# Optimization experiments

Measured on AMD Instinct MI355X. Metric: run time of the kernel, lower is better.

The kernel has to match this reference:

```python
import jax, jax.numpy as jnp
import numpy as np
import math

B, T, H, NH, E, W = 64, 256, 512, 8, 7, 5
DH = H // NH
NEG = -10000.0


def _ln(x, g, b, eps=1e-12):
    m = x.mean(-1, keepdims=True)
    v = ((x - m) ** 2).mean(-1, keepdims=True)
    return (x - m) / jnp.sqrt(v + eps) * g + b


def _attn(q_in, k_in, v_in, Wq, bq, Wk, bk, Wv, bv, bias):
    # q_in: [B,Tq,H], k_in/v_in: [B,Tk,H], bias broadcastable to [B,NH,Tq,Tk]
    Bq, Tq, _ = q_in.shape
    Tk = k_in.shape[1]
    q = (q_in @ Wq + bq).reshape(Bq, Tq, NH, DH)
    k = (k_in @ Wk + bk).reshape(Bq, Tk, NH, DH)
    v = (v_in @ Wv + bv).reshape(Bq, Tk, NH, DH)
    s = jnp.einsum('bqhd,bkhd->bhqk', q, k) / math.sqrt(DH) + bias
    p = jax.nn.softmax(s, axis=-1)
    ctx = jnp.einsum('bhqk,bkhd->bqhd', p, v)
    return ctx.reshape(Bq, Tq, H)


def _make_mask_biases(lengths, speakers):
    # Vectorized equivalents of get_ext_att_mask (additive -10000 biases).
    j = jnp.arange(T)[None, :, None]          # query position
    k = jnp.arange(T)[None, None, :]          # key position
    L = lengths[:, None, None]                # [B,1,1]
    row = j < L                               # valid query rows
    col = k < L                               # valid key cols
    # global: [B,1,1,T], key validity only
    bias_g = ((1.0 - col.astype(jnp.float32)) * NEG)[:, None, :, :]  # j dim acts as the size-1 axis
    # local: sliding window of width W (odd): |j-k| <= W//2, within length
    m_l = row & col & (jnp.abs(j - k) <= (W // 2))
    # intra: same-speaker keys for valid rows (columns NOT trimmed, per source)
    sp_j = speakers[:, :, None]
    sp_k = speakers[:, None, :]
    m_intra = row & (sp_k == sp_j)
    # inter: different-speaker keys for valid rows, columns trimmed to length
    m_inter = row & (sp_k != sp_j) & col
    to_bias = lambda m: ((1.0 - m.astype(jnp.float32)) * NEG)[:, None, :, :]
    return bias_g, to_bias(m_l), to_bias(m_intra), to_bias(m_inter)


def _forward(x, lengths, speakers, emo_table,
             t_Wq, t_bq, t_Wk, t_bk, t_Wv, t_bv, t_Wo, t_bo, t_ln_g, t_ln_b,
             b_Wq, b_bq, b_Wk, b_bk, b_Wv, b_bv, b_Wo, b_bo,
             W1, b1, ln2_g, ln2_b, W2):
    # Tendency attention: utterances attend to the E emotion embeddings (BertAttention)
    emo = jnp.broadcast_to(emo_table[None], (B, E, H))
    ctx = _attn(x, emo, emo, t_Wq, t_bq, t_Wk, t_bk, t_Wv, t_bv, 0.0)
    h_t = _ln(ctx @ t_Wo + t_bo + x, t_ln_g, t_ln_b)
    # Four masked self-attention branches (EmotionAttention: attn + dense, no LN)
    biases = _make_mask_biases(lengths, speakers)
    outs = []
    for i in range(4):
        c = _attn(h_t, h_t, h_t, b_Wq[i], b_bq[i], b_Wk[i], b_bk[i],
                  b_Wv[i], b_bv[i], biases[i])
        outs.append(c @ b_Wo[i] + b_bo[i])
    cat = jnp.concatenate(outs, axis=-1)          # [B,T,4H]
    h_e = _ln(cat @ W1 + b1 + h_t, ln2_g, ln2_b)  # fuse branches + residual + LN
    return h_e @ W2                                # transform2 (no bias)


def setup_inputs():
    key = jax.random.key(0)
    ks = jax.random.split(key, 16)
    nrm = lambda k, shape: jax.random.normal(k, shape, dtype=jnp.float32) * 0.02
    z = lambda *s: jnp.zeros(s, jnp.float32)
    o = lambda *s: jnp.ones(s, jnp.float32)
    return {
        'x': jax.random.normal(ks[0], (B, T, H), dtype=jnp.float32),
        'lengths': jax.random.randint(ks[1], (B,), T // 2, T + 1),
        'speakers': jax.random.randint(ks[2], (B, T), 0, 2),
        'emo_table': nrm(ks[3], (E, H)),
        't_Wq': nrm(ks[4], (H, H)), 't_bq': z(H),
        't_Wk': nrm(ks[5], (H, H)), 't_bk': z(H),
        't_Wv': nrm(ks[6], (H, H)), 't_bv': z(H),
        't_Wo': nrm(ks[7], (H, H)), 't_bo': z(H),
        't_ln_g': o(H), 't_ln_b': z(H),
        'b_Wq': nrm(ks[8], (4, H, H)), 'b_bq': z(4, H),
        'b_Wk': nrm(ks[9], (4, H, H)), 'b_bk': z(4, H),
        'b_Wv': nrm(ks[10], (4, H, H)), 'b_bv': z(4, H),
        'b_Wo': nrm(ks[11], (4, H, H)), 'b_bo': z(4, H),
        'W1': nrm(ks[12], (4 * H, H)), 'b1': z(H),
        'ln2_g': o(H), 'ln2_b': z(H),
        'W2': nrm(ks[13], (H, H)),
    }


def reference(x, lengths, speakers, emo_table,
              t_Wq, t_bq, t_Wk, t_bk, t_Wv, t_bv, t_Wo, t_bo, t_ln_g, t_ln_b,
              b_Wq, b_bq, b_Wk, b_bk, b_Wv, b_bv, b_Wo, b_bo,
              W1, b1, ln2_g, ln2_b, W2):
    return _forward(x, lengths, speakers, emo_table,
                    t_Wq, t_bq, t_Wk, t_bk, t_Wv, t_bv, t_Wo, t_bo, t_ln_g, t_ln_b,
                    b_Wq, b_bq, b_Wk, b_bk, b_Wv, b_bv, b_Wo, b_bo,
                    W1, b1, ln2_g, ln2_b, W2)
```

## Files before the change

### kernel.cpp

```cpp
#include <hip/hip_runtime.h>

#define B_  64
#define T_  256
#define H_  512
#define NH_ 8
#define DH_ 64
#define M_  16384
#define SL  262144

typedef float  f32x4 __attribute__((ext_vector_type(4)));
typedef float  f32x2 __attribute__((ext_vector_type(2)));
typedef __bf16 b16x8 __attribute__((ext_vector_type(8)));
typedef __bf16 b16x4 __attribute__((ext_vector_type(4)));
typedef __bf16 b16x2 __attribute__((ext_vector_type(2)));

__device__ __forceinline__ void gload16(const void* g, void* l) {
  __builtin_amdgcn_global_load_lds((const __attribute__((address_space(1))) void*)g,
                                   (__attribute__((address_space(3))) void*)l, 16, 0, 0);
}

__global__ __launch_bounds__(256) void cvt_f32_bf16_k(const float* __restrict__ in,
                                                      __bf16* __restrict__ out) {
  size_t i = ((size_t)blockIdx.x * 256 + threadIdx.x) * 4;
  f32x4 v = *(const f32x4*)(in + i);
  b16x4 o;
  o[0] = (__bf16)v[0]; o[1] = (__bf16)v[1]; o[2] = (__bf16)v[2]; o[3] = (__bf16)v[3];
  *(b16x4*)(out + i) = o;
}

struct TP15 { const float* src[15]; int slot[15]; float scl[15]; };
__global__ __launch_bounds__(256) void transpose_cvt15(TP15 p, __bf16* __restrict__ wT) {
  __shared__ float tile[32][33];
  const float* in = p.src[blockIdx.z];
  __bf16* out = wT + (size_t)p.slot[blockIdx.z] * SL;
  const float scl = p.scl[blockIdx.z];
  int c0 = blockIdx.x * 32, r0 = blockIdx.y * 32;
  int tx = threadIdx.x & 31, ty = threadIdx.x >> 5;
  for (int yy = ty; yy < 32; yy += 8)
    tile[yy][tx] = in[(size_t)(r0 + yy) * 512 + c0 + tx];
  __syncthreads();
  for (int yy = ty; yy < 32; yy += 8)
    out[(size_t)(c0 + yy) * 512 + r0 + tx] = (__bf16)(tile[tx][yy] * scl);
}

__global__ __launch_bounds__(256) void transpose_cvt(const float* __restrict__ in,
                                                     __bf16* __restrict__ out, int R, int C) {
  __shared__ float tile[32][33];
  int c0 = blockIdx.x * 32, r0 = blockIdx.y * 32;
  int tx = threadIdx.x & 31, ty = threadIdx.x >> 5;
  for (int yy = ty; yy < 32; yy += 8)
    tile[yy][tx] = in[(size_t)(r0 + yy) * C + c0 + tx];
  __syncthreads();
  for (int yy = ty; yy < 32; yy += 8)
    out[(size_t)(c0 + yy) * R + r0 + tx] = (__bf16)tile[tx][yy];
}

__global__ __launch_bounds__(512) void emo_kv(const float* __restrict__ emo,
                                              const float* __restrict__ Wk, const float* __restrict__ bk,
                                              const float* __restrict__ Wv, const float* __restrict__ bv,
                                              float* __restrict__ kout, float* __restrict__ vout) {
  int e = blockIdx.x, n = threadIdx.x;
  const float* W = blockIdx.y ? Wv : Wk;
  const float* bb = blockIdx.y ? bv : bk;
  float* o = blockIdx.y ? vout : kout;
  float acc = 0.f;
  for (int kk = 0; kk < 512; ++kk) acc += emo[e * 512 + kk] * W[kk * 512 + n];
  o[e * 512 + n] = acc + bb[n];
}

__global__ __launch_bounds__(512) void sentprep(const float* __restrict__ Wq,
                                                const float* __restrict__ bq,
                                                const float* __restrict__ Wo,
                                                const float* __restrict__ kemo,
                                                const float* __restrict__ vemo,
                                                __bf16* __restrict__ Wqk_bf,
                                                __bf16* __restrict__ VWo_bf,
                                                float* __restrict__ sbias) {
  const int he = blockIdx.x, h = he / 7, e = he % 7;
  const int t = threadIdx.x;
  const float* kp = kemo + e * 512 + h * 64;
  const float* wqr = Wq + (size_t)t * 512 + h * 64;
  float a = 0.f;
#pragma unroll 8
  for (int d = 0; d < 64; ++d) a += wqr[d] * kp[d];
  Wqk_bf[he * 512 + t] = (__bf16)(a * 0.125f);
  const float* vp = vemo + e * 512 + h * 64;
  float v = 0.f;
#pragma unroll 8
  for (int d = 0; d < 64; ++d) v += vp[d] * Wo[(size_t)(h * 64 + d) * 512 + t];
  VWo_bf[t * 64 + h * 8 + e] = (__bf16)v;
  if (e == 0) VWo_bf[t * 64 + h * 8 + 7] = (__bf16)0.f;
  if (t == 0) {
    float s = 0.f;
    for (int d = 0; d < 64; ++d) s += bq[h * 64 + d] * kp[d];
    sbias[he] = s * 0.125f;
  }
}

__global__ __launch_bounds__(512) void sentpad(__bf16* __restrict__ Wqk_bf,
                                               float* __restrict__ sbias) {
  int r = 56 + blockIdx.x;
  Wqk_bf[r * 512 + threadIdx.x] = (__bf16)0.f;
  if (threadIdx.x == 0) sbias[r] = 0.f;
}

__global__ __launch_bounds__(512) void concat_qk_bias(const float* __restrict__ bq,
                                                      const float* __restrict__ bk,
                                                      float* __restrict__ out) {
  int i = blockIdx.x, t = threadIdx.x;
  int base = (i >> 1) * 2048 + (i & 1) * 1024;
  out[base + t]       = bq[i * 512 + t];
  out[base + 512 + t] = bk[i * 512 + t] * 0.125f;
}

__global__ __launch_bounds__(256) void bias2_p1(const float* __restrict__ bo,
                                                const float* __restrict__ W1,
                                                float* __restrict__ partial) {
  int p = blockIdx.x, t = threadIdx.x;
  float a0 = 0.f, a1 = 0.f;
  for (int g = p * 128; g < p * 128 + 128; ++g) {
    float bg = bo[g];
    a0 += bg * W1[(size_t)g * 512 + t];
    a1 += bg * W1[(size_t)g * 512 + 256 + t];
  }
  partial[p * 512 + t] = a0;
  partial[p * 512 + 256 + t] = a1;
}

__global__ __launch_bounds__(256) void bias2_p2(const float* __restrict__ b1,
                                                const float* __restrict__ partial,
                                                float* __restrict__ out) {
  int o = blockIdx.x * 256 + threadIdx.x;
  float acc = b1[o];
#pragma unroll
  for (int p = 0; p < 16; ++p) acc += partial[p * 512 + o];
  out[o] = acc;
}

template<bool OB, int BM, int SW>
__global__ __launch_bounds__(512, 2) void gemm32(const __bf16* __restrict__ A,
                                                 const __bf16* __restrict__ Bt,
                                                 const float* __restrict__ bias,
                                                 void* __restrict__ Cv,
                                                 int N, int K, int lda, int ldc) {
  __shared__ __attribute__((aligned(16))) __bf16 As[2][256 * 32];
  __shared__ __attribute__((aligned(16))) __bf16 Bs[2][128 * 32];
  const int gx = gridDim.x;
  const int bid = blockIdx.y * gx + blockIdx.x;
  int bx, by;
  if (SW == 0) {
    const int nwg = gx * gridDim.y;
    const int cpx = nwg >> 3;
    const int swz = (bid & 7) * cpx + (bid >> 3);
    bx = swz % gx; by = swz / gx;
  } else {
    const int gxc = gx >> 3;
    const int u = bid >> 3, c = bid & 7;
    bx = c * gxc + u % gxc;
    by = u / gxc;
  }
  const int tid = threadIdx.x, lane = tid & 63, wid = tid >> 6;
  const int wr = wid >> 2, wc = wid & 3;
  const int m0 = by * 256, n0 = bx * 128;
  const int l15 = lane & 15, l16 = lane >> 4;
  const int ra = tid >> 2;
  const int xsl = (tid & 3) ^ ((ra >> 1) & 3);
  const int nt = K >> 5;
  f32x4 acc[8][2] = {};

#define STAGE32(buf, k0)                                                             \
  { char* aw = (char*)&As[buf][0];                                                   \
    char* bw = (char*)&Bs[buf][0];                                                   \
    gload16(A + (size_t)(m0 + ra) * lda + (k0) + xsl * 8, aw + tid * 16);            \
    gload16(A + (size_t)(m0 + 128 + ra) * lda + (k0) + xsl * 8, aw + (512 + tid) * 16); \
    gload16(Bt + (size_t)(n0 + ra) * K + (k0) + xsl * 8, bw + tid * 16); }

#define CMP32(buf)                                                                   \
  { const char* Ac = (const char*)&As[buf][0];                                       \
    const char* Bc = (const char*)&Bs[buf][0];                                       \
    const int swb = ((l16 ^ ((l15 >> 1) & 3)) << 4);                                 \
    b16x8 af[8], bf[2];                                                              \
    _Pragma("unroll")                                                                \
    for (int m = 0; m < 8; ++m)                                                      \
      af[m] = *(const b16x8*)(Ac + (wr * 128 + m * 16 + l15) * 64 + swb);            \
    _Pragma("unroll")                                                                \
    for (int n = 0; n < 2; ++n)                                                      \
      bf[n] = *(const b16x8*)(Bc + (wc * 32 + n * 16 + l15) * 64 + swb);             \
    __builtin_amdgcn_s_setprio(1);                                                   \
    _Pragma("unroll")                                                                \
    for (int m = 0; m < 8; ++m)                                                      \
      _Pragma("unroll")                                                              \
      for (int n = 0; n < 2; ++n)                                                    \
        acc[m][n] = __builtin_amdgcn_mfma_f32_16x16x32_bf16(af[m], bf[n], acc[m][n], 0, 0, 0); \
    __builtin_amdgcn_s_setprio(0); }

  STAGE32(0, 0);
  int cur = 0;
  for (int t = 0; t < nt; ++t) {
    if (t + 1 < nt) {
      STAGE32(cur ^ 1, (t + 1) * 32);
      asm volatile("s_waitcnt vmcnt(3)" ::: "memory");
    } else {
      asm volatile("s_waitcnt vmcnt(0)" ::: "memory");
    }
    __builtin_amdgcn_s_barrier();
    CMP32(cur);
    asm volatile("s_waitcnt lgkmcnt(0)" ::: "memory");
    __builtin_amdgcn_s_barrier();
    cur ^= 1;
  }
#undef STAGE32
#undef CMP32

  const int rb = m0 + wr * 128 + l16 * 4;
  const int cb = n0 + wc * 32 + l15;
#pragma unroll
  for (int n = 0; n < 2; ++n) {
    int gc = cb + n * 16;
    float bc = (BM == 1) ? bias[gc] : 0.0f;
#pragma unroll
    for (int m = 0; m < 8; ++m) {
#pragma unroll
      for (int rr = 0; rr < 4; ++rr) {
        int gr = rb + m * 16 + rr;
        float val = acc[m][n][rr] + ((BM == 2) ? bias[gr] : bc);
        if (OB) ((__bf16*)Cv)[(size_t)gr * ldc + gc] = (__bf16)val;
        else    ((float*)Cv)[(size_t)gr * ldc + gc] = val;
      }
    }
  }
}

template<bool OB, int BM, int SW>
__global__ __launch_bounds__(256) void gemm_bt64(const __bf16* __restrict__ A,
                                                 const __bf16* __restrict__ Bt,
                                                 const float* __restrict__ bias,
                                                 void* __restrict__ Cv,
                                                 int N, int K, int lda, int ldc,
                                                 size_t zA, size_t zB, size_t zC) {
  __shared__ __attribute__((aligned(16))) __bf16 As[128 * 32];
  __shared__ __attribute__((aligned(16))) __bf16 Bs[64 * 32];
  A  += (size_t)blockIdx.z * zA;
  Bt += (size_t)blockIdx.z * zB;
  char* Cb = (char*)Cv + (size_t)blockIdx.z * zC * (OB ? 2 : 4);
  const int gx = gridDim.x;
  const int bid = blockIdx.y * gx + blockIdx.x;
  int bx, by;
  if (SW == 0) {
    const int nwg = gx * gridDim.y;
    const int cpx = nwg >> 3;
    const int swz = (bid & 7) * cpx + (bid >> 3);
    bx = swz % gx; by = swz / gx;
  } else {
    const int gxc = gx >> 3;
    const int u = bid >> 3, c = bid & 7;
    bx = c * gxc + u % gxc;
    by = u / gxc;
  }
  const int tid = threadIdx.x, lane = tid & 63, wid = tid >> 6;
  const int m0 = by * 128, n0 = bx * 64;
  const int l15 = lane & 15, l16 = lane >> 4;
  const int r0 = tid >> 2, o0 = (tid & 3) * 8;
  const __bf16* a0 = A + (size_t)(m0 + r0) * lda + o0;
  const __bf16* a1 = A + (size_t)(m0 + 64 + r0) * lda + o0;
  const __bf16* bp0 = Bt + (size_t)(n0 + r0) * K + o0;
  char* AsW = (char*)As + wid * 1024;
  char* BsW = (char*)Bs + wid * 1024;
  f32x4 acc[2][4] = {};
  for (int k0 = 0; k0 < K; k0 += 32) {
    gload16(a0 + k0, AsW);
    gload16(a1 + k0, AsW + 4096);
    gload16(bp0 + k0, BsW);
    __syncthreads();
    b16x8 af[2], bf[4];
#pragma unroll
    for (int m = 0; m < 2; ++m) af[m] = *(const b16x8*)&As[(wid * 32 + m * 16 + l15) * 32 + l16 * 8];
#pragma unroll
    for (int n = 0; n < 4; ++n) bf[n] = *(const b16x8*)&Bs[(n * 16 + l15) * 32 + l16 * 8];
#pragma unroll
    for (int m = 0; m < 2; ++m)
#pragma unroll
      for (int n = 0; n < 4; ++n)
        acc[m][n] = __builtin_amdgcn_mfma_f32_16x16x32_bf16(af[m], bf[n], acc[m][n], 0, 0, 0);
    __syncthreads();
  }
  const int rbase = m0 + wid * 32 + l16 * 4;
  const int cb = n0 + l15;
#pragma unroll
  for (int n = 0; n < 4; ++n) {
    int gc = cb + n * 16;
    float bc = (BM == 1) ? bias[gc] : 0.0f;
#pragma unroll
    for (int m = 0; m < 2; ++m) {
#pragma unroll
      for (int rr = 0; rr < 4; ++rr) {
        int gr = rbase + m * 16 + rr;
        float val = acc[m][n][rr] + ((BM == 2) ? bias[gr] : bc);
        if (OB) ((__bf16*)Cb)[(size_t)gr * ldc + gc] = (__bf16)val;
        else    ((float*)Cb)[(size_t)gr * ldc + gc] = val;
      }
    }
  }
}

__global__ __launch_bounds__(256) void softmax7(const float* __restrict__ scores,
                                                __bf16* __restrict__ P) {
  int idx = blockIdx.x * 256 + threadIdx.x;
  int m = idx >> 3, h = idx & 7;
  const float* s = scores + (size_t)m * 64 + h * 7;
  float v[7], mx = -3.4e38f;
#pragma unroll
  for (int e = 0; e < 7; ++e) { v[e] = s[e]; mx = fmaxf(mx, v[e]); }
  float sum = 0.f;
#pragma unroll
  for (int e = 0; e < 7; ++e) { v[e] = __expf(v[e] - mx); sum += v[e]; }
  float inv = 1.f / sum;
  __bf16* o = P + (size_t)m * 64 + h * 8;
#pragma unroll
  for (int e = 0; e < 7; ++e) o[e] = (__bf16)(v[e] * inv);
  o[7] = (__bf16)0.f;
}

__global__ __launch_bounds__(256) void ln1_bf(const __bf16* __restrict__ pre,
                                              const float* __restrict__ res,
                                              const float* __restrict__ g,
                                              const float* __restrict__ bt,
                                              __bf16* __restrict__ ob) {
  int row = blockIdx.x, t = threadIdx.x;
  size_t base = (size_t)row * 512;
  b16x2 p2 = *(const b16x2*)(pre + base + 2 * t);
  f32x2 r2 = *(const f32x2*)(res + base + 2 * t);
  float v0 = (float)p2[0] + r2[0];
  float v1 = (float)p2[1] + r2[1];
  float s = v0 + v1, q = v0 * v0 + v1 * v1;
#pragma unroll
  for (int off = 32; off; off >>= 1) { s += __shfl_xor(s, off); q += __shfl_xor(q, off); }
  __shared__ float ls[4], lq[4];
  int wid = t >> 6, lane = t & 63;
  if (lane == 0) { ls[wid] = s; lq[wid] = q; }
  __syncthreads();
  s = ls[0] + ls[1] + ls[2] + ls[3];
  q = lq[0] + lq[1] + lq[2] + lq[3];
  float mean = s * (1.f / 512.f);
  float var = q * (1.f / 512.f) - mean * mean;
  float rstd = rsqrtf(fmaxf(var, 0.f) + 1e-12f);
  b16x2 o;
  o[0] = (__bf16)((v0 - mean) * rstd * g[2 * t] + bt[2 * t]);
  o[1] = (__bf16)((v1 - mean) * rstd * g[2 * t + 1] + bt[2 * t + 1]);
  *(b16x2*)(ob + base + 2 * t) = o;
}

__global__ __launch_bounds__(256) void ln2_bb(const __bf16* __restrict__ pre,
                                              const __bf16* __restrict__ res,
                                              const float* __restrict__ g,
                                              const float* __restrict__ bt,
                                              __bf16* __restrict__ ob) {
  int row = blockIdx.x, t = threadIdx.x;
  size_t base = (size_t)row * 512;
  b16x2 p2 = *(const b16x2*)(pre + base + 2 * t);
  b16x2 r2 = *(const b16x2*)(res + base + 2 * t);
  float v0 = (float)p2[0] + (float)r2[0];
  float v1 = (float)p2[1] + (float)r2[1];
  float s = v0 + v1, q = v0 * v0 + v1 * v1;
#pragma unroll
  for (int off = 32; off; off >>= 1) { s += __shfl_xor(s, off); q += __shfl_xor(q, off); }
  __shared__ float ls[4], lq[4];
  int wid = t >> 6, lane = t & 63;
  if (lane == 0) { ls[wid] = s; lq[wid] = q; }
  __syncthreads();
  s = ls[0] + ls[1] + ls[2] + ls[3];
  q = lq[0] + lq[1] + lq[2] + lq[3];
  float mean = s * (1.f / 512.f);
  float var = q * (1.f / 512.f) - mean * mean;
  float rstd = rsqrtf(fmaxf(var, 0.f) + 1e-12f);
  b16x2 o;
  o[0] = (__bf16)((v0 - mean) * rstd * g[2 * t] + bt[2 * t]);
  o[1] = (__bf16)((v1 - mean) * rstd * g[2 * t + 1] + bt[2 * t + 1]);
  *(b16x2*)(ob + base + 2 * t) = o;
}

template<int PAIR>
__global__ __launch_bounds__(256, 4) void attn_branch(const __bf16* __restrict__ qk,
                                                      const __bf16* __restrict__ vt,
                                                      __bf16* __restrict__ ctx,
                                                      const int* __restrict__ lengths,
                                                      const int* __restrict__ speakers) {
  __shared__ __attribute__((aligned(16))) __bf16 Ks[256 * 64];
  __shared__ __attribute__((aligned(16))) __bf16 Ps[32 * 264];
  __shared__ float redS[2][32];
  __shared__ int spk[256];
  const int sqk = 2048, so = 2048;
  const int tid = threadIdx.x, lane = tid & 63, wid = tid >> 6;
  const int l15 = lane & 15, l16 = lane >> 4;
  const int bh = blockIdx.x, z = blockIdx.y;
  const int BR = PAIR * 2 + z;
  const int b = bh >> 3, h = bh & 7;
  const int wq = wid & 1, wk = wid >> 1;
  const int mh = wid & 1, nh = wid >> 1;
  const __bf16* qp = qk + z * 1024;
  const __bf16* kp = qp + 512;
  const __bf16* vb2 = vt + (size_t)(BR * 512 + h * DH_) * M_ + b * T_;
  __bf16* ctxp = ctx + (size_t)BR * 512;
  const __bf16 CB = (__bf16)10000.0f, mCB = (__bf16)(-10000.0f), ZB = (__bf16)0.0f, OB1 = (__bf16)1.0f;
  const float CBF = (float)CB;
  const float MSTAR = (BR == 1) ? 16.0f : CBF + 16.0f;

  {
    const size_t kb0 = (size_t)(b * T_) * sqk + h * DH_;
    const int rsub = lane >> 3, slot = lane & 7;
#pragma unroll
    for (int j = 0; j < 8; ++j) {
      int row = (j * 4 + wid) * 8 + rsub;
      gload16(kp + kb0 + (size_t)row * sqk + ((slot ^ (row & 7)) * 8),
              (char*)Ks + (j * 4 + wid) * 1024);
    }
  }
  spk[tid] = speakers[b * T_ + tid];
  __syncthreads();
  const int L = lengths[b];

  b16x8 af0, af1;
  {
    const __bf16* qr = qp + (size_t)(b * T_ + wq * 16 + l15) * sqk + h * DH_;
    af0 = *(const b16x8*)(qr + l16 * 8);
    af1 = *(const b16x8*)(qr + 32 + l16 * 8);
  }

  for (int qc = 0; qc < 8; ++qc) {
    const int q0 = qc * 32;
    b16x8 afU = {};
    if (BR != 1 && l16 == 0) {
      int jA = q0 + wq * 16 + l15;
      bool rv = jA < L;
      afU[0] = rv ? OB1 : ZB;
      afU[1] = (rv && spk[jA]) ? OB1 : ZB;
      afU[2] = (BR == 0) ? OB1 : (rv ? ZB : OB1);
    }

    f32x4 sa[4][2] = {};
#pragma unroll
    for (int kc = 0; kc < 4; ++kc) {
#pragma unroll
      for (int nn = 0; nn < 2; ++nn) {
        int krw = kc * 64 + wk * 32 + nn * 16 + l15;
        b16x8 b0 = *(const b16x8*)((char*)Ks + krw * 128 + ((l16 ^ (krw & 7)) * 16));
        sa[kc][nn] = __builtin_amdgcn_mfma_f32_16x16x32_bf16(af0, b0, sa[kc][nn], 0, 0, 0);
        b16x8 b1 = *(const b16x8*)((char*)Ks + krw * 128 + (((4 + l16) ^ (krw & 7)) * 16));
        sa[kc][nn] = __builtin_amdgcn_mfma_f32_16x16x32_bf16(af1, b1, sa[kc][nn], 0, 0, 0);
        if (BR != 1) {
          b16x8 w = {};
          if (l16 == 0) {
            bool cv = krw < L;
            int sc = spk[krw];
            if (BR == 0) {
              w[2] = cv ? CB : ZB;
            } else if (BR == 2) {
              w[0] = sc ? ZB : CB;
              w[1] = sc ? CB : mCB;
              w[2] = CB;
            } else {
              w[0] = (cv && sc) ? CB : ZB;
              w[1] = cv ? (sc ? mCB : CB) : ZB;
              w[2] = CB;
            }
          }
          sa[kc][nn] = __builtin_amdgcn_mfma_f32_16x16x32_bf16(afU, w, sa[kc][nn], 0, 0, 0);
        }
      }
    }

    if (qc + 1 < 8) {
      const __bf16* qr = qp + (size_t)(b * T_ + (qc + 1) * 32 + wq * 16 + l15) * sqk + h * DH_;
      af0 = *(const b16x8*)(qr + l16 * 8);
      af1 = *(const b16x8*)(qr + 32 + l16 * 8);
    }

    const int rloc = wq * 16 + l16 * 4;
    float sm[4];
#pragma unroll
    for (int rr = 0; rr < 4; ++rr) {
      const int j = q0 + rloc + rr;
      const bool rv = j < L;
      float s = 0.f;
#pragma unroll
      for (int kc = 0; kc < 4; ++kc)
#pragma unroll
        for (int nn = 0; nn < 2; ++nn) {
          float v = sa[kc][nn][rr];
          if (BR == 1) {
            int c = kc * 64 + wk * 32 + nn * 16 + l15;
            int dj = j - c;
            bool ok = (c < L) && (dj <= 2) && (dj >= -2);
            v += (ok || !rv) ? 0.0f : -10000.0f;
          }
          float e = __expf(v - MSTAR);
          sa[kc][nn][rr] = e;
          s += e;
        }
      s += __shfl_xor(s, 1); s += __shfl_xor(s, 2); s += __shfl_xor(s, 4); s += __shfl_xor(s, 8);
      sm[rr] = s;
    }
#pragma unroll
    for (int rr = 0; rr < 4; ++rr) {
      if (l15 == 0) redS[wk][rloc + rr] = sm[rr];
#pragma unroll
      for (int kc = 0; kc < 4; ++kc)
#pragma unroll
        for (int nn = 0; nn < 2; ++nn)
          Ps[(rloc + rr) * 264 + kc * 64 + wk * 32 + nn * 16 + l15] = (__bf16)sa[kc][nn][rr];
    }
    __syncthreads();

    f32x4 oa[2] = {};
#pragma unroll
    for (int kt = 0; kt < 8; ++kt) {
      b16x8 afp = *(const b16x8*)(Ps + (mh * 16 + l15) * 264 + kt * 32 + l16 * 8);
#pragma unroll
      for (int n = 0; n < 2; ++n) {
        int d = nh * 32 + n * 16 + l15;
        b16x8 bfr = *(const b16x8*)(vb2 + (size_t)d * M_ + kt * 32 + l16 * 8);
        oa[n] = __builtin_amdgcn_mfma_f32_16x16x32_bf16(afp, bfr, oa[n], 0, 0, 0);
      }
    }
#pragma unroll
    for (int rr = 0; rr < 4; ++rr) {
      int row = mh * 16 + l16 * 4 + rr;
      float rinv = 1.0f / (redS[0][row] + redS[1][row]);
#pragma unroll
      for (int n = 0; n < 2; ++n)
        ctxp[(size_t)(b * T_ + q0 + row) * so + h * DH_ + nh * 32 + n * 16 + l15]
            = (__bf16)(oa[n][rr] * rinv);
    }
    __syncthreads();
  }
}

extern "C" void kernel_launch(void* const* d_in, const int* in_sizes, int n_in,
                              void* d_out, int out_size, void* d_ws, size_t ws_size,
                              hipStream_t stream) {
  const float* x        = (const float*)d_in[0];
  const int*   lengths  = (const int*)d_in[1];
  const int*   speakers = (const int*)d_in[2];
  const float* emo      = (const float*)d_in[3];
  const float* t_Wq = (const float*)d_in[4];
  const float* t_bq = (const float*)d_in[5];
  const float* t_Wk = (const float*)d_in[6];
  const float* t_bk = (const float*)d_in[7];
  const float* t_Wv = (const float*)d_in[8];
  const float* t_bv = (const float*)d_in[9];
  const float* t_Wo = (const float*)d_in[10];
  const float* t_bo = (const float*)d_in[11];
  const float* t_ln_g = (const float*)d_in[12];
  const float* t_ln_b = (const float*)d_in[13];
  const float* b_Wq = (const float*)d_in[14];
  const float* b_bq = (const float*)d_in[15];
  const float* b_Wk = (const float*)d_in[16];
  const float* b_bk = (const float*)d_in[17];
  const float* b_Wv = (const float*)d_in[18];
  const float* b_bv = (const float*)d_in[19];
  const float* b_Wo = (const float*)d_in[20];
  const float* b_bo = (const float*)d_in[21];
  const float* W1   = (const float*)d_in[22];
  const float* b1   = (const float*)d_in[23];
  const float* ln2_g = (const float*)d_in[24];
  const float* ln2_b = (const float*)d_in[25];
  const float* W2   = (const float*)d_in[26];

  if (ws_size < 232314880) return;

  char* ws = (char*)d_ws;
  __bf16* wT      = (__bf16*)(ws);
  __bf16* bWo_bf  = (__bf16*)(ws + 9437184);
  __bf16* Btbig   = (__bf16*)(ws + 11534336);
  float*  qkbias  = (float*)(ws + 13631488);
  float*  bias2   = (float*)(ws + 13647872);
  float*  kemo    = (float*)(ws + 13649920);
  float*  vemo    = (float*)(ws + 13664256);
  __bf16* Wqk_bf  = (__bf16*)(ws + 13678592);
  __bf16* VWo_bf  = (__bf16*)(ws + 13744128);
  float*  sbias   = (float*)(ws + 13809664);
  __bf16* htb     = (__bf16*)(ws + 13908224);
  __bf16* qkb2    = (__bf16*)(ws + 30685440);
  __bf16* vtb_all = (__bf16*)(ws + 97794304);
  __bf16* ctxa    = (__bf16*)(ws + 164903168);
  __bf16* xb      = (__bf16*)(ws + 164903168);
  float*  partial = (float*)(ws + 30685440);
  float*  scores  = (float*)(ws + 30685440);
  __bf16* Pmat    = (__bf16*)(ws + 30685440 + 4194304);
  __bf16* sctx    = (__bf16*)(ws + 30685440 + 8388608);
  __bf16* tmpb    = qkb2;
  __bf16* heb     = (__bf16*)(ws + 47462656);

  cvt_f32_bf16_k<<<dim3(8192), 256, 0, stream>>>(x, xb);
  cvt_f32_bf16_k<<<dim3(1024), 256, 0, stream>>>(b_Wo, bWo_bf);
  {
    TP15 p;
    const float* srcs[13] = {b_Wq, b_Wq + SL, b_Wq + 2 * SL, b_Wq + 3 * SL,
                             b_Wk, b_Wk + SL, b_Wk + 2 * SL, b_Wk + 3 * SL,
                             b_Wv, b_Wv + SL, b_Wv + 2 * SL, b_Wv + 3 * SL,
                             W2};
    const int slots[13] = {2, 4, 6, 8, 3, 5, 7, 9, 10, 11, 12, 13, 0};
    for (int i = 0; i < 13; ++i) {
      p.src[i] = srcs[i]; p.slot[i] = slots[i];
      p.scl[i] = (i >= 4 && i < 8) ? 0.125f : 1.0f;
    }
    for (int i = 13; i < 15; ++i) { p.src[i] = W2; p.slot[i] = 0; p.scl[i] = 1.0f; }
    transpose_cvt15<<<dim3(16, 16, 13), 256, 0, stream>>>(p, wT);
  }
  transpose_cvt<<<dim3(16, 64), 256, 0, stream>>>(W1, wT + 14 * SL, 2048, 512);
  emo_kv<<<dim3(7, 2), 512, 0, stream>>>(emo, t_Wk, t_bk, t_Wv, t_bv, kemo, vemo);
  concat_qk_bias<<<dim3(4), 512, 0, stream>>>(b_bq, b_bk, qkbias);
  bias2_p1<<<dim3(16), 256, 0, stream>>>(b_bo, W1, partial);
  bias2_p2<<<dim3(2), 256, 0, stream>>>(b1, partial, bias2);
  sentprep<<<dim3(56), 512, 0, stream>>>(t_Wq, t_bq, t_Wo, kemo, vemo, Wqk_bf, VWo_bf, sbias);
  sentpad<<<dim3(8), 512, 0, stream>>>(Wqk_bf, sbias);
  gemm_bt64<true, 0, 0><<<dim3(8, 4, 4), 256, 0, stream>>>(wT + 14 * SL, bWo_bf, nullptr, Btbig,
                                                           512, 512, 2048, 2048, 512, SL, 512);

  gemm_bt64<false, 1, 0><<<dim3(1, 128), 256, 0, stream>>>(xb, Wqk_bf, sbias, scores,
                                                           64, 512, 512, 64, 0, 0, 0);
  softmax7<<<dim3(512), 256, 0, stream>>>(scores, Pmat);
  gemm_bt64<true, 1, 0><<<dim3(8, 128), 256, 0, stream>>>(Pmat, VWo_bf, t_bo, sctx,
                                                          512, 64, 64, 512, 0, 0, 0);
  ln1_bf<<<dim3(16384), 256, 0, stream>>>(sctx, x, t_ln_g, t_ln_b, htb);

  gemm32<true, 2, 1><<<dim3(128, 8), 512, 0, stream>>>(wT + 10 * SL, htb, b_bv,
                                                       vtb_all, 16384, 512, 512, 16384);

  for (int p = 0; p < 2; ++p) {
    gemm32<true, 1, 0><<<dim3(16, 64), 512, 0, stream>>>(htb, wT + (2 + 4 * p) * SL, qkbias + p * 2048,
                                                         qkb2, 2048, 512, 512, 2048);
    dim3 ag(512, 2);
    if (p == 0) attn_branch<0><<<ag, 256, 0, stream>>>(qkb2, vtb_all, ctxa, lengths, speakers);
    else        attn_branch<1><<<ag, 256, 0, stream>>>(qkb2, vtb_all, ctxa, lengths, speakers);
  }

  gemm32<true, 1, 0><<<dim3(4, 64), 512, 0, stream>>>(ctxa, Btbig, bias2, tmpb, 512, 2048, 2048, 512);
  ln2_bb<<<dim3(16384), 256, 0, stream>>>(tmpb, htb, ln2_g, ln2_b, heb);
  gemm32<false, 0, 0><<<dim3(4, 64), 512, 0, stream>>>(heb, wT + 0 * SL, nullptr, (float*)d_out, 512, 512, 512, 512);
}
```

Measured before the change: 510.7 us.

## Give each wave full key rows in branch attention to drop block barriers

Restructures the branch attention kernel so each wave owns 16 query rows across all 256 keys and computes the full softmax row sum itself. This removes the cross-wave reduction through shared memory and both per-iteration __syncthreads, and gives each wave a private P buffer. Each wave now computes all 64 output head dims, so it reads V for the full head and holds 16 score accumulators in registers. The launch_bounds occupancy hint is dropped, which may raise register pressure and lower occupancy.

```diff
diff --git a/kernel.cpp b/kernel.cpp
--- a/kernel.cpp
+++ b/kernel.cpp
@@ -380,14 +380,13 @@
 }
 
 template<int PAIR>
-__global__ __launch_bounds__(256, 4) void attn_branch(const __bf16* __restrict__ qk,
-                                                      const __bf16* __restrict__ vt,
-                                                      __bf16* __restrict__ ctx,
-                                                      const int* __restrict__ lengths,
-                                                      const int* __restrict__ speakers) {
+__global__ __launch_bounds__(256) void attn_branch(const __bf16* __restrict__ qk,
+                                                   const __bf16* __restrict__ vt,
+                                                   __bf16* __restrict__ ctx,
+                                                   const int* __restrict__ lengths,
+                                                   const int* __restrict__ speakers) {
   __shared__ __attribute__((aligned(16))) __bf16 Ks[256 * 64];
-  __shared__ __attribute__((aligned(16))) __bf16 Ps[32 * 264];
-  __shared__ float redS[2][32];
+  __shared__ __attribute__((aligned(16))) __bf16 Ps[4][16 * 264];
   __shared__ int spk[256];
   const int sqk = 2048, so = 2048;
   const int tid = threadIdx.x, lane = tid & 63, wid = tid >> 6;
@@ -395,8 +394,6 @@
   const int bh = blockIdx.x, z = blockIdx.y;
   const int BR = PAIR * 2 + z;
   const int b = bh >> 3, h = bh & 7;
-  const int wq = wid & 1, wk = wid >> 1;
-  const int mh = wid & 1, nh = wid >> 1;
   const __bf16* qp = qk + z * 1024;
   const __bf16* kp = qp + 512;
   const __bf16* vb2 = vt + (size_t)(BR * 512 + h * DH_) * M_ + b * T_;
@@ -418,120 +415,109 @@
   spk[tid] = speakers[b * T_ + tid];
   __syncthreads();
   const int L = lengths[b];
+  __bf16* PsW = &Ps[wid][0];
 
   b16x8 af0, af1;
   {
-    const __bf16* qr = qp + (size_t)(b * T_ + wq * 16 + l15) * sqk + h * DH_;
+    const __bf16* qr = qp + (size_t)(b * T_ + wid * 16 + l15) * sqk + h * DH_;
     af0 = *(const b16x8*)(qr + l16 * 8);
     af1 = *(const b16x8*)(qr + 32 + l16 * 8);
   }
 
-  for (int qc = 0; qc < 8; ++qc) {
-    const int q0 = qc * 32;
+  for (int it = 0; it < 4; ++it) {
+    const int q0 = it * 64 + wid * 16;
     b16x8 afU = {};
     if (BR != 1 && l16 == 0) {
-      int jA = q0 + wq * 16 + l15;
+      int jA = q0 + l15;
       bool rv = jA < L;
       afU[0] = rv ? OB1 : ZB;
       afU[1] = (rv && spk[jA]) ? OB1 : ZB;
       afU[2] = (BR == 0) ? OB1 : (rv ? ZB : OB1);
     }
 
-    f32x4 sa[4][2] = {};
-#pragma unroll
-    for (int kc = 0; kc < 4; ++kc) {
-#pragma unroll
-      for (int nn = 0; nn < 2; ++nn) {
-        int krw = kc * 64 + wk * 32 + nn * 16 + l15;
-        b16x8 b0 = *(const b16x8*)((char*)Ks + krw * 128 + ((l16 ^ (krw & 7)) * 16));
-        sa[kc][nn] = __builtin_amdgcn_mfma_f32_16x16x32_bf16(af0, b0, sa[kc][nn], 0, 0, 0);
-        b16x8 b1 = *(const b16x8*)((char*)Ks + krw * 128 + (((4 + l16) ^ (krw & 7)) * 16));
-        sa[kc][nn] = __builtin_amdgcn_mfma_f32_16x16x32_bf16(af1, b1, sa[kc][nn], 0, 0, 0);
-        if (BR != 1) {
-          b16x8 w = {};
-          if (l16 == 0) {
-            bool cv = krw < L;
-            int sc = spk[krw];
-            if (BR == 0) {
-              w[2] = cv ? CB : ZB;
-            } else if (BR == 2) {
-              w[0] = sc ? ZB : CB;
-              w[1] = sc ? CB : mCB;
-              w[2] = CB;
-            } else {
-              w[0] = (cv && sc) ? CB : ZB;
-              w[1] = cv ? (sc ? mCB : CB) : ZB;
-              w[2] = CB;
-            }
+    f32x4 sa[16];
+#pragma unroll
+    for (int nn = 0; nn < 16; ++nn) {
+      int krw = nn * 16 + l15;
+      b16x8 b0 = *(const b16x8*)((char*)Ks + krw * 128 + ((l16 ^ (krw & 7)) * 16));
+      f32x4 zv = {};
+      zv = __builtin_amdgcn_mfma_f32_16x16x32_bf16(af0, b0, zv, 0, 0, 0);
+      b16x8 b1 = *(const b16x8*)((char*)Ks + krw * 128 + (((4 + l16) ^ (krw & 7)) * 16));
+      sa[nn] = __builtin_amdgcn_mfma_f32_16x16x32_bf16(af1, b1, zv, 0, 0, 0);
+      if (BR != 1) {
+        b16x8 w = {};
+        if (l16 == 0) {
+          bool cv = krw < L;
+          int sc = spk[krw];
+          if (BR == 0) {
+            w[2] = cv ? CB : ZB;
+          } else if (BR == 2) {
+            w[0] = sc ? ZB : CB;
+            w[1] = sc ? CB : mCB;
+            w[2] = CB;
+          } else {
+            w[0] = (cv && sc) ? CB : ZB;
+            w[1] = cv ? (sc ? mCB : CB) : ZB;
+            w[2] = CB;
           }
-          sa[kc][nn] = __builtin_amdgcn_mfma_f32_16x16x32_bf16(afU, w, sa[kc][nn], 0, 0, 0);
         }
+        sa[nn] = __builtin_amdgcn_mfma_f32_16x16x32_bf16(afU, w, sa[nn], 0, 0, 0);
       }
     }
 
-    if (qc + 1 < 8) {
-      const __bf16* qr = qp + (size_t)(b * T_ + (qc + 1) * 32 + wq * 16 + l15) * sqk + h * DH_;
+    if (it + 1 < 4) {
+      const __bf16* qr = qp + (size_t)(b * T_ + (it + 1) * 64 + wid * 16 + l15) * sqk + h * DH_;
       af0 = *(const b16x8*)(qr + l16 * 8);
       af1 = *(const b16x8*)(qr + 32 + l16 * 8);
     }
 
-    const int rloc = wq * 16 + l16 * 4;
-    float sm[4];
+    float rinv[4];
 #pragma unroll
     for (int rr = 0; rr < 4; ++rr) {
-      const int j = q0 + rloc + rr;
+      const int j = q0 + l16 * 4 + rr;
       const bool rv = j < L;
       float s = 0.f;
 #pragma unroll
-      for (int kc = 0; kc < 4; ++kc)
-#pragma unroll
-        for (int nn = 0; nn < 2; ++nn) {
-          float v = sa[kc][nn][rr];
-          if (BR == 1) {
-            int c = kc * 64 + wk * 32 + nn * 16 + l15;
-            int dj = j - c;
-            bool ok = (c < L) && (dj <= 2) && (dj >= -2);
-            v += (ok || !rv) ? 0.0f : -10000.0f;
-          }
-          float e = __expf(v - MSTAR);
-          sa[kc][nn][rr] = e;
-          s += e;
+      for (int nn = 0; nn < 16; ++nn) {
+        float v = sa[nn][rr];
+        if (BR == 1) {
+          int c = nn * 16 + l15;
+          int dj = j - c;
+          bool ok = (c < L) && (dj <= 2) && (dj >= -2);
+          v += (ok || !rv) ? 0.0f : -10000.0f;
         }
+        float e = __expf(v - MSTAR);
+        sa[nn][rr] = e;
+        s += e;
+      }
       s += __shfl_xor(s, 1); s += __shfl_xor(s, 2); s += __shfl_xor(s, 4); s += __shfl_xor(s, 8);
-      sm[rr] = s;
-    }
-#pragma unroll
-    for (int rr = 0; rr < 4; ++rr) {
-      if (l15 == 0) redS[wk][rloc + rr] = sm[rr];
-#pragma unroll
-      for (int kc = 0; kc < 4; ++kc)
-#pragma unroll
-        for (int nn = 0; nn < 2; ++nn)
-          Ps[(rloc + rr) * 264 + kc * 64 + wk * 32 + nn * 16 + l15] = (__bf16)sa[kc][nn][rr];
-    }
-    __syncthreads();
-
-    f32x4 oa[2] = {};
+      rinv[rr] = 1.0f / s;
+    }
+
+#pragma unroll
+    for (int rr = 0; rr < 4; ++rr)
+#pragma unroll
+      for (int nn = 0; nn < 16; ++nn)
+        PsW[(l16 * 4 + rr) * 264 + nn * 16 + l15] = (__bf16)sa[nn][rr];
+
+    f32x4 oa[4] = {};
 #pragma unroll
     for (int kt = 0; kt < 8; ++kt) {
-      b16x8 afp = *(const b16x8*)(Ps + (mh * 16 + l15) * 264 + kt * 32 + l16 * 8);
-#pragma unroll
-      for (int n = 0; n < 2; ++n) {
-        int d = nh * 32 + n * 16 + l15;
-        b16x8 bfr = *(const b16x8*)(vb2 + (size_t)d * M_ + kt * 32 + l16 * 8);
+      b16x8 afp = *(const b16x8*)&PsW[l15 * 264 + kt * 32 + l16 * 8];
+#pragma unroll
+      for (int n = 0; n < 4; ++n) {
+        b16x8 bfr = *(const b16x8*)(vb2 + (size_t)(n * 16 + l15) * M_ + kt * 32 + l16 * 8);
         oa[n] = __builtin_amdgcn_mfma_f32_16x16x32_bf16(afp, bfr, oa[n], 0, 0, 0);
       }
     }
 #pragma unroll
     for (int rr = 0; rr < 4; ++rr) {
-      int row = mh * 16 + l16 * 4 + rr;
-      float rinv = 1.0f / (redS[0][row] + redS[1][row]);
-#pragma unroll
-      for (int n = 0; n < 2; ++n)
-        ctxp[(size_t)(b * T_ + q0 + row) * so + h * DH_ + nh * 32 + n * 16 + l15]
-            = (__bf16)(oa[n][rr] * rinv);
-    }
-    __syncthreads();
+      int row = q0 + l16 * 4 + rr;
+#pragma unroll
+      for (int n = 0; n < 4; ++n)
+        ctxp[(size_t)(b * T_ + row) * so + h * DH_ + n * 16 + l15]
+            = (__bf16)(oa[n][rr] * rinv[rr]);
+    }
   }
 }
 
```

Measured after the change: 576.5 us. 12.9% more time.
